# Kernel tuning notes

Measured on AMD Instinct MI355X. Metric: run time of the kernel, lower is better.

Reference implementation:

```python
import jax, jax.numpy as jnp
import numpy as np

NUM_HEADS = 16
HEAD_DIM = 128
WINDOW = 512
ROPE_BASE = 10000.0


def _rope_tables(seq_len, head_dim, dtype=jnp.float32):
    # rotate_dim == head_dim (rope_proportion=1.0)
    inv_freq = 1.0 / (ROPE_BASE ** (jnp.arange(0, head_dim, 2, dtype=jnp.float32) / head_dim))
    freqs = jnp.arange(seq_len, dtype=jnp.float32)[:, None] * inv_freq[None, :]  # (S, D/2)
    return jnp.cos(freqs).astype(dtype), jnp.sin(freqs).astype(dtype)


def _apply_rope(x, cos, sin):
    # x: (B, H, S, D); interleaved-pair RoPE matching torch reference
    x1 = x[..., 0::2]
    x2 = x[..., 1::2]
    cos = cos[None, None]  # (1,1,S,D/2)
    sin = sin[None, None]
    re = x1 * cos - x2 * sin
    ro = x1 * sin + x2 * cos
    out = jnp.stack([re, ro], axis=-1)  # (B,H,S,D/2,2)
    return out.reshape(x.shape)


def setup_inputs() -> dict:
    key = jax.random.key(0)
    ks = jax.random.split(key, 5)
    B, S, D = 2, 2048, 2048
    std = 0.02
    x = jax.random.normal(ks[0], (B, S, D), dtype=jnp.float32)
    Wq = std * jax.random.normal(ks[1], (D, D), dtype=jnp.float32)
    Wk = std * jax.random.normal(ks[2], (D, D), dtype=jnp.float32)
    Wv = std * jax.random.normal(ks[3], (D, D), dtype=jnp.float32)
    Wo = std * jax.random.normal(ks[4], (D, D), dtype=jnp.float32)
    return {"x": x, "Wq": Wq, "Wk": Wk, "Wv": Wv, "Wo": Wo}


def reference(x, Wq, Wk, Wv, Wo):
    B, S, D = x.shape
    H, Dh = NUM_HEADS, HEAD_DIM
    scale = Dh ** -0.5

    def to_heads(t):
        return t.reshape(B, S, H, Dh).transpose(0, 2, 1, 3)  # (B,H,S,Dh)

    q = to_heads(x @ Wq.T)
    k = to_heads(x @ Wk.T)
    v = to_heads(x @ Wv.T)

    cos, sin = _rope_tables(S, Dh)
    q = _apply_rope(q, cos, sin)
    k = _apply_rope(k, cos, sin)

    # sliding-window causal mask: keep if 0 <= row-col < WINDOW
    pos = jnp.arange(S)
    diff = pos[:, None] - pos[None, :]
    keep = (diff >= 0) & (diff < WINDOW)  # (S,S) bool

    scores = jnp.einsum('bhsd,bhtd->bhst', q, k) * scale
    scores = jnp.where(keep[None, None], scores, jnp.finfo(scores.dtype).min)
    attn = jax.nn.softmax(scores, axis=-1)
    out = jnp.einsum('bhst,bhtd->bhsd', attn, v)  # (B,H,S,Dh)
    out = out.transpose(0, 2, 1, 3).reshape(B, S, D)
    return out @ Wo.T
```

## Files before the change

### kernel.cpp

```cpp
#include <hip/hip_runtime.h>
#include <cstdint>
#include <cstddef>

typedef __bf16 bf16x8 __attribute__((ext_vector_type(8)));
typedef float f32x4 __attribute__((ext_vector_type(4)));
typedef float f32x16 __attribute__((ext_vector_type(16)));
typedef unsigned int u32x2v __attribute__((ext_vector_type(2)));
typedef unsigned short u16;

constexpr int S_LEN  = 2048;
constexpr int DMODEL = 2048;
constexpr int NHEAD  = 16;
constexpr int HDIM   = 128;
constexpr int WIN    = 512;

#define AS1 __attribute__((address_space(1)))
#define AS3 __attribute__((address_space(3)))

__device__ __forceinline__ u16 f2bf(float f) {
  union { float ff; uint32_t u; } a; a.ff = f;
  return (u16)((a.u + 0x7fffu + ((a.u >> 16) & 1u)) >> 16);
}

__device__ __forceinline__ uint32_t cvtpk(float lo, float hi) {
  uint32_t r;
  asm("v_cvt_pk_bf16_f32 %0, %1, %2" : "=v"(r) : "v"(lo), "v"(hi));
  return r;
}

__global__ void cvt_all(const float* __restrict__ x,  const float* __restrict__ wq,
                        const float* __restrict__ wk, const float* __restrict__ wv,
                        const float* __restrict__ wo,
                        u16* __restrict__ xb,  u16* __restrict__ wqb,
                        u16* __restrict__ wkb, u16* __restrict__ wvb,
                        u16* __restrict__ wob) {
  const int total = 6291456;
  int i = blockIdx.x * blockDim.x + threadIdx.x;
  const int stride = gridDim.x * blockDim.x;
  for (; i < total; i += stride) {
    const int r = i >> 20;
    const float* src; u16* dst; int off;
    if (r < 2)       { src = x;  dst = xb;  off = i; }
    else if (r == 2) { src = wq; dst = wqb; off = i - (2 << 20); }
    else if (r == 3) { src = wk; dst = wkb; off = i - (3 << 20); }
    else if (r == 4) { src = wv; dst = wvb; off = i - (4 << 20); }
    else             { src = wo; dst = wob; off = i - (5 << 20); }
    float4 v = reinterpret_cast<const float4*>(src)[off];
    uint2 pk;
    pk.x = (uint32_t)f2bf(v.x) | ((uint32_t)f2bf(v.y) << 16);
    pk.y = (uint32_t)f2bf(v.z) | ((uint32_t)f2bf(v.w) << 16);
    reinterpret_cast<uint2*>(dst)[off] = pk;
  }
}

__global__ void rope_kernel(float* __restrict__ rc, float* __restrict__ rs) {
  const int i = blockIdx.x * blockDim.x + threadIdx.x;
  const int s = i >> 6, f = i & 63;
  const double inv = exp(-(double)f * (log(10000.0) / 64.0));
  const double a = (double)s * inv;
  rc[i] = (float)cos(a);
  rs[i] = (float)sin(a);
}

__global__ __launch_bounds__(256, 4)
void gemm_qkv(const u16* __restrict__ A,
              const u16* __restrict__ wqb, const u16* __restrict__ wkb,
              const u16* __restrict__ wvb,
              u16* __restrict__ qout, u16* __restrict__ kout, u16* __restrict__ vtout,
              const float* __restrict__ rc, const float* __restrict__ rs) {
  constexpr int K = DMODEL;
  constexpr int BK = 64;
  __shared__ __align__(16) u16 As[128 * BK];
  __shared__ __align__(16) u16 Bs[128 * BK];

  const int lin = blockIdx.x;
  const int g = (lin & 7) * 192 + (lin >> 3);
  const int mt = g / 48, ctg = g % 48;
  const int region = ctg >> 4;
  const u16* Bw = region == 0 ? wqb : region == 1 ? wkb : wvb;
  const int brow = mt * 128;
  const int bcol = (ctg & 15) * 128;

  const int tid = threadIdx.x;
  const int w = tid >> 6, lane = tid & 63;
  const int lr = lane & 15, lk = lane >> 4;
  const int wm = w >> 1, wn = w & 1;

  f32x4 acc[4][4] = {};

  const int st_row = w * 32 + (lane >> 3);
  const int st_col = (lane & 7) * 8;
  const u16* Ag = A  + (size_t)(brow + st_row) * K + st_col;
  const u16* Bg = Bw + (size_t)(bcol + st_row) * K + st_col;
  u16* AsW = As + w * 32 * BK;
  u16* BsW = Bs + w * 32 * BK;

  for (int k0 = 0; k0 < K; k0 += BK) {
#pragma unroll
    for (int i = 0; i < 4; ++i)
      __builtin_amdgcn_global_load_lds(
          (const AS1 void*)(Ag + (size_t)i * 8 * K + k0),
          (AS3 void*)(AsW + i * 8 * BK), 16, 0, 0);
#pragma unroll
    for (int i = 0; i < 4; ++i)
      __builtin_amdgcn_global_load_lds(
          (const AS1 void*)(Bg + (size_t)i * 8 * K + k0),
          (AS3 void*)(BsW + i * 8 * BK), 16, 0, 0);
    __syncthreads();
#pragma unroll
    for (int kc = 0; kc < 2; ++kc) {
      bf16x8 a[4], b[4];
#pragma unroll
      for (int m = 0; m < 4; ++m)
        a[m] = *reinterpret_cast<const bf16x8*>(&As[(wm * 64 + m * 16 + lr) * BK + kc * 32 + lk * 8]);
#pragma unroll
      for (int n = 0; n < 4; ++n)
        b[n] = *reinterpret_cast<const bf16x8*>(&Bs[(wn * 64 + n * 16 + lr) * BK + kc * 32 + lk * 8]);
#pragma unroll
      for (int m = 0; m < 4; ++m)
#pragma unroll
        for (int n = 0; n < 4; ++n)
          acc[m][n] = __builtin_amdgcn_mfma_f32_16x16x32_bf16(a[m], b[n], acc[m][n], 0, 0, 0);
    }
    __syncthreads();
  }

  if (region == 2) {
#pragma unroll
    for (int m = 0; m < 4; ++m) {
      const int gm0 = brow + wm * 64 + m * 16 + lk * 4;
      const int b = gm0 >> 11, s = gm0 & 2047;
#pragma unroll
      for (int n = 0; n < 4; ++n) {
        const int gn = bcol + wn * 64 + n * 16 + lr;
        const int h = gn >> 7, dh = gn & 127;
        uint2 pk;
        pk.x = (uint32_t)f2bf(acc[m][n][0]) | ((uint32_t)f2bf(acc[m][n][1]) << 16);
        pk.y = (uint32_t)f2bf(acc[m][n][2]) | ((uint32_t)f2bf(acc[m][n][3]) << 16);
        *reinterpret_cast<uint2*>(&vtout[((size_t)((b * NHEAD + h) * HDIM + dh)) * S_LEN + s]) = pk;
      }
    }
  } else {
    u16* QK = region == 0 ? qout : kout;
#pragma unroll
    for (int m = 0; m < 4; ++m) {
      const int gm0 = brow + wm * 64 + m * 16 + lk * 4;
      const int b = gm0 >> 11, s0 = gm0 & 2047;
#pragma unroll
      for (int n = 0; n < 4; ++n) {
        const int gn = bcol + wn * 64 + n * 16 + lr;
        const int h = gn >> 7, dh = gn & 127;
        const int fi = dh >> 1;
        const bool ev = (dh & 1) == 0;
#pragma unroll
        for (int j = 0; j < 4; ++j) {
          float v = acc[m][n][j];
          float pp = __shfl_xor(v, 1, 64);
          const float c  = rc[(s0 + j) * 64 + fi];
          const float sn = rs[(s0 + j) * 64 + fi];
          float oo = ev ? (v * c - pp * sn) : (pp * sn + v * c);
          if (region == 0) oo *= 0.08838834764831845f;
          QK[((size_t)(b * NHEAD + h) * S_LEN + (s0 + j)) * HDIM + dh] = f2bf(oo);
        }
      }
    }
  }
}

__global__ __launch_bounds__(256, 4)
void gemm_o(const u16* __restrict__ A, const u16* __restrict__ Bw,
            float* __restrict__ O) {
  constexpr int K = DMODEL;
  constexpr int BK = 64;
  __shared__ __align__(16) u16 As[128 * BK];
  __shared__ __align__(16) u16 Bs[128 * BK];

  const int lin = blockIdx.x;
  const int g = (lin & 7) * 64 + (lin >> 3);
  const int mt = g / 16, ct = g % 16;
  const int brow = mt * 128;
  const int bcol = ct * 128;

  const int tid = threadIdx.x;
  const int w = tid >> 6, lane = tid & 63;
  const int lr = lane & 15, lk = lane >> 4;
  const int wm = w >> 1, wn = w & 1;

  f32x4 acc[4][4] = {};

  const int st_row = w * 32 + (lane >> 3);
  const int st_col = (lane & 7) * 8;
  const u16* Ag = A  + (size_t)(brow + st_row) * K + st_col;
  const u16* Bg = Bw + (size_t)(bcol + st_row) * K + st_col;
  u16* AsW = As + w * 32 * BK;
  u16* BsW = Bs + w * 32 * BK;

  for (int k0 = 0; k0 < K; k0 += BK) {
#pragma unroll
    for (int i = 0; i < 4; ++i)
      __builtin_amdgcn_global_load_lds(
          (const AS1 void*)(Ag + (size_t)i * 8 * K + k0),
          (AS3 void*)(AsW + i * 8 * BK), 16, 0, 0);
#pragma unroll
    for (int i = 0; i < 4; ++i)
      __builtin_amdgcn_global_load_lds(
          (const AS1 void*)(Bg + (size_t)i * 8 * K + k0),
          (AS3 void*)(BsW + i * 8 * BK), 16, 0, 0);
    __syncthreads();
#pragma unroll
    for (int kc = 0; kc < 2; ++kc) {
      bf16x8 a[4], b[4];
#pragma unroll
      for (int m = 0; m < 4; ++m)
        a[m] = *reinterpret_cast<const bf16x8*>(&As[(wm * 64 + m * 16 + lr) * BK + kc * 32 + lk * 8]);
#pragma unroll
      for (int n = 0; n < 4; ++n)
        b[n] = *reinterpret_cast<const bf16x8*>(&Bs[(wn * 64 + n * 16 + lr) * BK + kc * 32 + lk * 8]);
#pragma unroll
      for (int m = 0; m < 4; ++m)
#pragma unroll
        for (int n = 0; n < 4; ++n)
          acc[m][n] = __builtin_amdgcn_mfma_f32_16x16x32_bf16(a[m], b[n], acc[m][n], 0, 0, 0);
    }
    __syncthreads();
  }

#pragma unroll
  for (int m = 0; m < 4; ++m) {
    const int gm0 = brow + wm * 64 + m * 16 + lk * 4;
#pragma unroll
    for (int n = 0; n < 4; ++n) {
      const int gn = bcol + wn * 64 + n * 16 + lr;
#pragma unroll
      for (int j = 0; j < 4; ++j)
        O[(size_t)(gm0 + j) * DMODEL + gn] = acc[m][n][j];
    }
  }
}

__global__ __launch_bounds__(256, 2)
void swa3_kernel(const u16* __restrict__ Qp, const u16* __restrict__ Kp,
                 const u16* __restrict__ Vt, u16* __restrict__ AO) {
  __shared__ __align__(16) u16 Ksh[2][64 * 128];
  __shared__ __align__(16) u16 Vsh[2][128 * 64];

  const int lin = blockIdx.x + gridDim.x * blockIdx.y;
  const int slot = lin >> 3;
  const int bh = (lin & 7) * 4 + (slot >> 4);
  const int qt = slot & 15;

  const int w = threadIdx.x >> 6;
  const int lane = threadIdx.x & 63;
  const int lq = lane & 31, hi = lane >> 5;
  const int qb_blk = qt * 128;
  const int qw = qb_blk + w * 32;
  const int qq = qw + lq;

  const u16* Qb = Qp + (size_t)bh * S_LEN * HDIM;
  const u16* Kb = Kp + (size_t)bh * S_LEN * HDIM;
  const u16* Vb = Vt + (size_t)bh * HDIM * S_LEN;

  bf16x8 qf[8];
#pragma unroll
  for (int s = 0; s < 8; ++s)
    qf[s] = *reinterpret_cast<const bf16x8*>(&Qb[(size_t)qq * HDIM + s * 16 + hi * 8]);

  f32x16 ot[4] = {};
  float m = 0.f, lsum = 0.f;

  const int c_lo = (qb_blk >= WIN) ? qb_blk - WIN : 0;
  const int c_hi = qb_blk + 128;

  auto stage = [&](int buf, int kc) {
#pragma unroll
    for (int i = 0; i < 4; ++i) {
      const int u = i * 256 + w * 64 + lane;
      const int row = u >> 4, sl = (u & 15) ^ (row & 7);
      __builtin_amdgcn_global_load_lds(
          (const AS1 void*)(Kb + (size_t)(kc + row) * HDIM + sl * 8),
          (AS3 void*)(&Ksh[buf][(size_t)(i * 256 + w * 64) * 8]), 16, 0, 0);
    }
#pragma unroll
    for (int i = 0; i < 4; ++i) {
      const int u = i * 256 + w * 64 + lane;
      const int row = u >> 3, sl = (u & 7) ^ (row & 7);
      __builtin_amdgcn_global_load_lds(
          (const AS1 void*)(Vb + (size_t)row * S_LEN + kc + sl * 8),
          (AS3 void*)(&Vsh[buf][(size_t)(i * 256 + w * 64) * 8]), 16, 0, 0);
    }
  };

  int buf = 0;
  stage(0, c_lo);
  __syncthreads();

  for (int kc = c_lo; kc < c_hi; kc += 64, buf ^= 1) {
    if (kc + 64 < c_hi) stage(buf ^ 1, kc + 64);

#pragma unroll
    for (int half = 0; half < 2; ++half) {
      const int kch = kc + half * 32;
      if (kch > qw + 31 || kch < qw - 542) continue;

      f32x16 P = {};
#pragma unroll
      for (int s = 0; s < 8; ++s) {
        const int row = half * 32 + lq;
        const int byte = row * 256 + ((s * 32 + hi * 16) ^ ((row & 7) << 4));
        bf16x8 kf = *reinterpret_cast<const bf16x8*>(&Ksh[buf][byte >> 1]);
        P = __builtin_amdgcn_mfma_f32_32x32x16_bf16(kf, qf[s], P, 0, 0, 0);
      }

      const bool needmask = (kch + 32 > qw) || (qw + 31 - kch >= WIN);
      float p[16];
      float pmax = -1e30f;
#pragma unroll
      for (int r = 0; r < 16; ++r) {
        float v = P[r];
        if (needmask) {
          const int kk = kch + (r & 3) + ((r >> 2) << 3) + hi * 4;
          const bool keep = (qq >= kk) && (qq - kk < WIN);
          v = keep ? v : -1e30f;
        }
        p[r] = v;
        pmax = fmaxf(pmax, v);
      }

      if (__any(pmax - m > 8.f)) {
        const float rm = fmaxf(pmax, __shfl_xor(pmax, 32, 64));
        const float mnew = fmaxf(m, rm);
        const float alpha = __expf(m - mnew);
        lsum *= alpha;
#pragma unroll
        for (int dt = 0; dt < 4; ++dt)
#pragma unroll
          for (int r = 0; r < 16; ++r) ot[dt][r] *= alpha;
        m = mnew;
      }

      float ls = 0.f;
#pragma unroll
      for (int r = 0; r < 16; ++r) {
        p[r] = __expf(p[r] - m);
        ls += p[r];
      }
      lsum += ls;

      uint32_t W[8];
#pragma unroll
      for (int i = 0; i < 8; ++i) W[i] = cvtpk(p[2 * i], p[2 * i + 1]);
      u32x2v r02 = __builtin_amdgcn_permlane32_swap(W[0], W[2], false, false);
      u32x2v r13 = __builtin_amdgcn_permlane32_swap(W[1], W[3], false, false);
      u32x2v r46 = __builtin_amdgcn_permlane32_swap(W[4], W[6], false, false);
      u32x2v r57 = __builtin_amdgcn_permlane32_swap(W[5], W[7], false, false);

#pragma unroll
      for (int ks = 0; ks < 2; ++ks) {
        union { uint32_t u[4]; bf16x8 v; } pb;
        if (ks == 0) { pb.u[0] = r02[0]; pb.u[1] = r13[0]; pb.u[2] = r02[1]; pb.u[3] = r13[1]; }
        else         { pb.u[0] = r46[0]; pb.u[1] = r57[0]; pb.u[2] = r46[1]; pb.u[3] = r57[1]; }
#pragma unroll
        for (int dt = 0; dt < 4; ++dt) {
          const int d = dt * 32 + lq;
          const int byte = d * 128 + ((half * 64 + ks * 32 + hi * 16) ^ ((d & 7) << 4));
          bf16x8 vf = *reinterpret_cast<const bf16x8*>(&Vsh[buf][byte >> 1]);
          ot[dt] = __builtin_amdgcn_mfma_f32_32x32x16_bf16(vf, pb.v, ot[dt], 0, 0, 0);
        }
      }
    }
    __syncthreads();
  }

  const float lf = lsum + __shfl_xor(lsum, 32, 64);
  const float inv = 1.f / lf;
  const int b = bh >> 4, h = bh & 15;
  u16* Ob = AO + (size_t)(b * S_LEN + qq) * DMODEL + h * HDIM;
#pragma unroll
  for (int dt = 0; dt < 4; ++dt)
#pragma unroll
    for (int rq = 0; rq < 4; ++rq) {
      uint2 pk;
      pk.x = cvtpk(ot[dt][rq * 4 + 0] * inv, ot[dt][rq * 4 + 1] * inv);
      pk.y = cvtpk(ot[dt][rq * 4 + 2] * inv, ot[dt][rq * 4 + 3] * inv);
      *reinterpret_cast<uint2*>(&Ob[dt * 32 + rq * 8 + hi * 4]) = pk;
    }
}

extern "C" void kernel_launch(void* const* d_in, const int* in_sizes, int n_in,
                              void* d_out, int out_size, void* d_ws, size_t ws_size,
                              hipStream_t stream) {
  const float* x  = (const float*)d_in[0];
  const float* Wq = (const float*)d_in[1];
  const float* Wk = (const float*)d_in[2];
  const float* Wv = (const float*)d_in[3];
  const float* Wo = (const float*)d_in[4];
  float* out = (float*)d_out;

  u16* p = (u16*)d_ws;
  u16* xb  = p; p += (size_t)4096 * 2048;
  u16* wqb = p; p += (size_t)2048 * 2048;
  u16* wkb = p; p += (size_t)2048 * 2048;
  u16* wvb = p; p += (size_t)2048 * 2048;
  u16* wob = p; p += (size_t)2048 * 2048;
  u16* qb  = p; p += (size_t)32 * 2048 * 128;
  u16* kb  = p; p += (size_t)32 * 2048 * 128;
  u16* vtb = p; p += (size_t)32 * 128 * 2048;
  u16* aob = p; p += (size_t)4096 * 2048;
  float* rc = (float*)p;
  float* rs = rc + (size_t)2048 * 64;

  cvt_all<<<3072, 256, 0, stream>>>(x, Wq, Wk, Wv, Wo, xb, wqb, wkb, wvb, wob);
  rope_kernel<<<512, 256, 0, stream>>>(rc, rs);
  gemm_qkv<<<1536, 256, 0, stream>>>(xb, wqb, wkb, wvb, qb, kb, vtb, rc, rs);
  swa3_kernel<<<dim3(16, 32), 256, 0, stream>>>(qb, kb, vtb, aob);
  gemm_o<<<512, 256, 0, stream>>>(aob, wob, out);
}
```

Before: 247.5 us.

## Rewrite QKV GEMM with 128x192 tiles, 4-stage LDS pipeline, concatenated weights

Replaces the QKV projection GEMM with a 128x192-tile kernel that reads one concatenated [Wq;Wk;Wv] weight matrix. It uses a 4-deep ring of 32-wide K slices in LDS, filled by global_load_lds three stages ahead, with explicit vmcnt waits and raised MFMA priority. The goal is to hide global-load latency and improve reuse per tile, at the cost of more LDS, more registers and lower occupancy (launch bounds 2). gemm_o drops its swizzled block mapping for a plain 2D grid. The new kernel relies on wqb, wkb and wvb being contiguous in the workspace; that holds because the buffers are allocated back to back. Tiles that straddle the Q/K/V boundary are handled per fragment in the epilogue.

```diff
diff --git a/kernel.cpp b/kernel.cpp
--- a/kernel.cpp
+++ b/kernel.cpp
@@ -16,6 +16,8 @@
 
 #define AS1 __attribute__((address_space(1)))
 #define AS3 __attribute__((address_space(3)))
+#define BAR() do { asm volatile("" ::: "memory"); __builtin_amdgcn_s_barrier(); asm volatile("" ::: "memory"); } while (0)
+#define WAITVM(n) asm volatile("s_waitcnt vmcnt(" #n ")" ::: "memory")
 
 __device__ __forceinline__ u16 f2bf(float f) {
   union { float ff; uint32_t u; } a; a.ff = f;
@@ -62,129 +64,122 @@
   rs[i] = (float)sin(a);
 }
 
-__global__ __launch_bounds__(256, 4)
-void gemm_qkv(const u16* __restrict__ A,
-              const u16* __restrict__ wqb, const u16* __restrict__ wkb,
-              const u16* __restrict__ wvb,
-              u16* __restrict__ qout, u16* __restrict__ kout, u16* __restrict__ vtout,
-              const float* __restrict__ rc, const float* __restrict__ rs) {
+__global__ __launch_bounds__(256, 2)
+void gemm_qkv192(const u16* __restrict__ A, const u16* __restrict__ Bcat,
+                 u16* __restrict__ qout, u16* __restrict__ kout, u16* __restrict__ vtout,
+                 const float* __restrict__ rc, const float* __restrict__ rs) {
   constexpr int K = DMODEL;
-  constexpr int BK = 64;
-  __shared__ __align__(16) u16 As[128 * BK];
-  __shared__ __align__(16) u16 Bs[128 * BK];
-
-  const int lin = blockIdx.x;
-  const int g = (lin & 7) * 192 + (lin >> 3);
-  const int mt = g / 48, ctg = g % 48;
-  const int region = ctg >> 4;
-  const u16* Bw = region == 0 ? wqb : region == 1 ? wkb : wvb;
+  constexpr int NH = K / 32;
+  __shared__ __align__(16) u16 sm[4 * 10240];
+
+  const int ct = blockIdx.x, mt = blockIdx.y;
   const int brow = mt * 128;
-  const int bcol = (ctg & 15) * 128;
+  const int bcol = ct * 192;
 
   const int tid = threadIdx.x;
   const int w = tid >> 6, lane = tid & 63;
   const int lr = lane & 15, lk = lane >> 4;
   const int wm = w >> 1, wn = w & 1;
 
-  f32x4 acc[4][4] = {};
-
-  const int st_row = w * 32 + (lane >> 3);
-  const int st_col = (lane & 7) * 8;
-  const u16* Ag = A  + (size_t)(brow + st_row) * K + st_col;
-  const u16* Bg = Bw + (size_t)(bcol + st_row) * K + st_col;
-  u16* AsW = As + w * 32 * BK;
-  u16* BsW = Bs + w * 32 * BK;
-
-  for (int k0 = 0; k0 < K; k0 += BK) {
-#pragma unroll
-    for (int i = 0; i < 4; ++i)
-      __builtin_amdgcn_global_load_lds(
-          (const AS1 void*)(Ag + (size_t)i * 8 * K + k0),
-          (AS3 void*)(AsW + i * 8 * BK), 16, 0, 0);
-#pragma unroll
-    for (int i = 0; i < 4; ++i)
-      __builtin_amdgcn_global_load_lds(
-          (const AS1 void*)(Bg + (size_t)i * 8 * K + k0),
-          (AS3 void*)(BsW + i * 8 * BK), 16, 0, 0);
-    __syncthreads();
-#pragma unroll
-    for (int kc = 0; kc < 2; ++kc) {
-      bf16x8 a[4], b[4];
-#pragma unroll
-      for (int m = 0; m < 4; ++m)
-        a[m] = *reinterpret_cast<const bf16x8*>(&As[(wm * 64 + m * 16 + lr) * BK + kc * 32 + lk * 8]);
-#pragma unroll
-      for (int n = 0; n < 4; ++n)
-        b[n] = *reinterpret_cast<const bf16x8*>(&Bs[(wn * 64 + n * 16 + lr) * BK + kc * 32 + lk * 8]);
-#pragma unroll
-      for (int m = 0; m < 4; ++m)
-#pragma unroll
-        for (int n = 0; n < 4; ++n)
-          acc[m][n] = __builtin_amdgcn_mfma_f32_16x16x32_bf16(a[m], b[n], acc[m][n], 0, 0, 0);
-    }
-    __syncthreads();
-  }
-
-  if (region == 2) {
-#pragma unroll
-    for (int m = 0; m < 4; ++m) {
-      const int gm0 = brow + wm * 64 + m * 16 + lk * 4;
-      const int b = gm0 >> 11, s = gm0 & 2047;
-#pragma unroll
-      for (int n = 0; n < 4; ++n) {
-        const int gn = bcol + wn * 64 + n * 16 + lr;
-        const int h = gn >> 7, dh = gn & 127;
+  const u16* Ag = A    + (size_t)brow * K;
+  const u16* Bg = Bcat + (size_t)bcol * K;
+
+  f32x4 acc[4][6] = {};
+
+  auto stage = [&](int h) {
+    const int sb = (h & 3) * 10240;
+#pragma unroll
+    for (int i = 0; i < 2; ++i) {
+      const int u = i * 256 + tid;
+      const int rf = u >> 6, lkk = (u >> 4) & 3, lrr = u & 15;
+      const u16* src = Ag + (size_t)(rf * 16 + lrr) * K + h * 32 + lkk * 8;
+      __builtin_amdgcn_global_load_lds((const AS1 void*)src,
+          (AS3 void*)(&sm[sb + (i * 256 + w * 64) * 8]), 16, 0, 0);
+    }
+#pragma unroll
+    for (int i = 0; i < 3; ++i) {
+      const int u = i * 256 + tid;
+      const int cf = u >> 6, lkk = (u >> 4) & 3, lrr = u & 15;
+      const u16* src = Bg + (size_t)(cf * 16 + lrr) * K + h * 32 + lkk * 8;
+      __builtin_amdgcn_global_load_lds((const AS1 void*)src,
+          (AS3 void*)(&sm[sb + (512 + i * 256 + w * 64) * 8]), 16, 0, 0);
+    }
+  };
+
+  stage(0); stage(1); stage(2);
+  WAITVM(10);
+  BAR();
+
+  for (int h = 0; h < NH; ++h) {
+    const int sb = (h & 3) * 10240;
+    bf16x8 a[4], b[6];
+#pragma unroll
+    for (int mf = 0; mf < 4; ++mf)
+      a[mf] = *reinterpret_cast<const bf16x8*>(&sm[sb + (((wm * 4 + mf) * 4 + lk) * 16 + lr) * 8]);
+#pragma unroll
+    for (int nf = 0; nf < 6; ++nf)
+      b[nf] = *reinterpret_cast<const bf16x8*>(&sm[sb + (512 + ((wn * 6 + nf) * 4 + lk) * 16 + lr) * 8]);
+    if (h + 3 < NH) stage(h + 3);
+    BAR();
+    __builtin_amdgcn_s_setprio(1);
+#pragma unroll
+    for (int mf = 0; mf < 4; ++mf)
+#pragma unroll
+      for (int nf = 0; nf < 6; ++nf)
+        acc[mf][nf] = __builtin_amdgcn_mfma_f32_16x16x32_bf16(a[mf], b[nf], acc[mf][nf], 0, 0, 0);
+    __builtin_amdgcn_s_setprio(0);
+    if (h < NH - 3)       { WAITVM(10); }
+    else if (h == NH - 3) { WAITVM(5); }
+    else if (h == NH - 2) { WAITVM(0); }
+    BAR();
+  }
+
+#pragma unroll
+  for (int mf = 0; mf < 4; ++mf) {
+    const int gm0 = brow + wm * 64 + mf * 16 + lk * 4;
+    const int b_ = gm0 >> 11, s0 = gm0 & 2047;
+#pragma unroll
+    for (int nf = 0; nf < 6; ++nf) {
+      const int gn = bcol + wn * 96 + nf * 16 + lr;
+      const int reg = gn >> 11;
+      const int h = (gn >> 7) & 15, dh = gn & 127;
+      if (reg == 2) {
         uint2 pk;
-        pk.x = (uint32_t)f2bf(acc[m][n][0]) | ((uint32_t)f2bf(acc[m][n][1]) << 16);
-        pk.y = (uint32_t)f2bf(acc[m][n][2]) | ((uint32_t)f2bf(acc[m][n][3]) << 16);
-        *reinterpret_cast<uint2*>(&vtout[((size_t)((b * NHEAD + h) * HDIM + dh)) * S_LEN + s]) = pk;
-      }
-    }
-  } else {
-    u16* QK = region == 0 ? qout : kout;
-#pragma unroll
-    for (int m = 0; m < 4; ++m) {
-      const int gm0 = brow + wm * 64 + m * 16 + lk * 4;
-      const int b = gm0 >> 11, s0 = gm0 & 2047;
-#pragma unroll
-      for (int n = 0; n < 4; ++n) {
-        const int gn = bcol + wn * 64 + n * 16 + lr;
-        const int h = gn >> 7, dh = gn & 127;
+        pk.x = (uint32_t)f2bf(acc[mf][nf][0]) | ((uint32_t)f2bf(acc[mf][nf][1]) << 16);
+        pk.y = (uint32_t)f2bf(acc[mf][nf][2]) | ((uint32_t)f2bf(acc[mf][nf][3]) << 16);
+        *reinterpret_cast<uint2*>(&vtout[((size_t)((b_ * NHEAD + h) * HDIM + dh)) * S_LEN + s0]) = pk;
+      } else {
+        u16* QK = reg == 0 ? qout : kout;
         const int fi = dh >> 1;
         const bool ev = (dh & 1) == 0;
 #pragma unroll
         for (int j = 0; j < 4; ++j) {
-          float v = acc[m][n][j];
+          float v = acc[mf][nf][j];
           float pp = __shfl_xor(v, 1, 64);
           const float c  = rc[(s0 + j) * 64 + fi];
           const float sn = rs[(s0 + j) * 64 + fi];
           float oo = ev ? (v * c - pp * sn) : (pp * sn + v * c);
-          if (region == 0) oo *= 0.08838834764831845f;
-          QK[((size_t)(b * NHEAD + h) * S_LEN + (s0 + j)) * HDIM + dh] = f2bf(oo);
+          if (reg == 0) oo *= 0.08838834764831845f;
+          QK[((size_t)(b_ * NHEAD + h) * S_LEN + (s0 + j)) * HDIM + dh] = f2bf(oo);
         }
       }
     }
   }
 }
 
-__global__ __launch_bounds__(256, 4)
+__global__ __launch_bounds__(256, 2)
 void gemm_o(const u16* __restrict__ A, const u16* __restrict__ Bw,
             float* __restrict__ O) {
   constexpr int K = DMODEL;
   constexpr int BK = 64;
   __shared__ __align__(16) u16 As[128 * BK];
   __shared__ __align__(16) u16 Bs[128 * BK];
-
-  const int lin = blockIdx.x;
-  const int g = (lin & 7) * 64 + (lin >> 3);
-  const int mt = g / 16, ct = g % 16;
-  const int brow = mt * 128;
-  const int bcol = ct * 128;
-
   const int tid = threadIdx.x;
   const int w = tid >> 6, lane = tid & 63;
   const int lr = lane & 15, lk = lane >> 4;
   const int wm = w >> 1, wn = w & 1;
+  const int brow = blockIdx.y * 128;
+  const int bcol = blockIdx.x * 128;
 
   f32x4 acc[4][4] = {};
 
@@ -411,7 +406,7 @@
 
   cvt_all<<<3072, 256, 0, stream>>>(x, Wq, Wk, Wv, Wo, xb, wqb, wkb, wvb, wob);
   rope_kernel<<<512, 256, 0, stream>>>(rc, rs);
-  gemm_qkv<<<1536, 256, 0, stream>>>(xb, wqb, wkb, wvb, qb, kb, vtb, rc, rs);
+  gemm_qkv192<<<dim3(32, 32), 256, 0, stream>>>(xb, wqb, qb, kb, vtb, rc, rs);
   swa3_kernel<<<dim3(16, 32), 256, 0, stream>>>(qb, kb, vtb, aob);
-  gemm_o<<<512, 256, 0, stream>>>(aob, wob, out);
-}
+  gemm_o<<<dim3(16, 32), 256, 0, stream>>>(aob, wob, out);
+}
```

New measurement: 269.2 us. +8.8%, slower.
